# Performance work log

Measured on AMD Instinct MI355X. Metric: run time of the kernel, lower is better.

## Reference

```python
import math
import jax, jax.numpy as jnp
import numpy as np

TOP_K = 2
_GELU_C = math.sqrt(2.0 / math.pi)

def gelu_new(x):
    # NewGELU: tanh approximation identical to the torch module
    return 0.5 * x * (1.0 + jnp.tanh(_GELU_C * (x + 0.044715 * x * x * x)))

def setup_inputs() -> dict:
    key = jax.random.key(0)
    ks = jax.random.split(key, 6)
    B, T, C, E, H = 2, 2048, 1024, 8, 4096
    s_in = 1.0 / math.sqrt(C)
    s_hid = 1.0 / math.sqrt(H)
    return {
        "x": jax.random.normal(ks[0], (B, T, C), dtype=jnp.float32),
        "router_w": jax.random.normal(ks[1], (E, C), dtype=jnp.float32) * s_in,
        "w_fc": jax.random.normal(ks[2], (E, C, H), dtype=jnp.float32) * s_in,
        "b_fc": jax.random.normal(ks[3], (E, H), dtype=jnp.float32) * 0.02,
        "w_proj": jax.random.normal(ks[4], (E, H, C), dtype=jnp.float32) * s_hid,
        "b_proj": jax.random.normal(ks[5], (E, C), dtype=jnp.float32) * 0.02,
    }

def reference(x, router_w, w_fc, b_fc, w_proj, b_proj):
    B, T, C = x.shape
    E = router_w.shape[0]
    N = B * T
    xf = x.reshape(N, C)
    # Router: Linear(C, E, bias=False), softmax, top-k, renormalize
    logits = xf @ router_w.T                              # [N, E]
    probs = jax.nn.softmax(logits, axis=-1)
    topk_probs, topk_idx = jax.lax.top_k(probs, TOP_K)    # [N, K]
    topk_probs = topk_probs / jnp.sum(topk_probs, axis=-1, keepdims=True)
    # Dense combine weights: zero for unselected experts -> same math as
    # gather/FFN/index_add over selected tokens (dropout=0).
    combine = jnp.zeros((N, E), dtype=x.dtype).at[
        jnp.arange(N)[:, None], topk_idx].add(topk_probs)  # [N, E]
    # Expert FFN applied per expert (batched GEMMs)
    h = gelu_new(jnp.einsum('nc,ech->neh', xf, w_fc) + b_fc)      # [N, E, H]
    out = jnp.einsum('neh,ehc->nec', h, w_proj) + b_proj          # [N, E, C]
    y = jnp.einsum('nec,ne->nc', out, combine)                    # [N, C]
    return y.reshape(B, T, C)
```

## Files before the change

### kernel.cpp

```cpp
#include <hip/hip_runtime.h>


#define NTOK  4096
#define CDIM  1024
#define HDIM  4096
#define NEXP  8
#define NPC   9216
#define MAXMT 72
#define KB_C  32
#define KB_H  128
#define KSPLIT 2

#define FC_TOTAL (32 * MAXMT)
#define FC_CHUNK (FC_TOTAL / 8)
#define PJ_TOTAL (8 * MAXMT * KSPLIT)
#define PJ_CHUNK (PJ_TOTAL / 8)

typedef _Float16 half8 __attribute__((ext_vector_type(8)));
typedef float    f32x4 __attribute__((ext_vector_type(4)));

#define ASYNC_CP16(gp, lp)                                                         \
  __builtin_amdgcn_global_load_lds(                                                \
      (const __attribute__((address_space(1))) unsigned int*)(gp),                 \
      (__attribute__((address_space(3))) unsigned int*)(lp), 16, 0, 0)

#define STAGE(kb, LA, LB, BSTRIDE)                                                 \
  {                                                                                \
    const char* ga_ = gA0 + (size_t)(kb) * (NPC * 64) + soff;                      \
    const char* gb_ = gB0 + (size_t)(kb) * ((BSTRIDE) * 64) + soff;                \
    ASYNC_CP16(ga_,        LA);                                                    \
    ASYNC_CP16(ga_ + 1024, LA + 1024);                                             \
    ASYNC_CP16(gb_,        LB);                                                    \
    ASYNC_CP16(gb_ + 1024, LB + 1024);                                             \
  }

#define WAITV(N) asm volatile("s_waitcnt vmcnt(" #N ")" ::: "memory")
#define BAR()    __builtin_amdgcn_s_barrier()
#define SCHED0() __builtin_amdgcn_sched_barrier(0)

__device__ __forceinline__ void compute_step(
    const _Float16* __restrict__ AS, const _Float16* __restrict__ BS,
    int wm, int wn, int l16, int lq, f32x4 (&acc)[4][4])
{
    half8 af[4], bfv[4];
    #pragma unroll
    for (int i = 0; i < 4; ++i) af[i]  = *(const half8*)&AS[(wm + i * 16 + l16) * 32 + lq * 8];
    #pragma unroll
    for (int j = 0; j < 4; ++j) bfv[j] = *(const half8*)&BS[(wn + j * 16 + l16) * 32 + lq * 8];
    #pragma unroll
    for (int i = 0; i < 4; ++i)
        #pragma unroll
        for (int j = 0; j < 4; ++j)
            acc[i][j] = __builtin_amdgcn_mfma_f32_16x16x32_f16(af[i], bfv[j], acc[i][j], 0, 0, 0);
}

#define PIPE_LOOP(kb_beg, kb_end, BSTRIDE)                                         \
  {                                                                                \
    STAGE((kb_beg),     lA0, lB0, BSTRIDE);                                        \
    STAGE((kb_beg) + 1, lA1, lB1, BSTRIDE);                                        \
    for (int t = (kb_beg); t + 2 < (kb_end); t += 2) {                             \
        WAITV(4); BAR();                                                           \
        compute_step(As0, Bs0, wm, wn, l16, lq, acc);                              \
        SCHED0(); BAR();                                                           \
        STAGE(t + 2, lA0, lB0, BSTRIDE);                                           \
        WAITV(4); BAR();                                                           \
        compute_step(As1, Bs1, wm, wn, l16, lq, acc);                              \
        SCHED0(); BAR();                                                           \
        STAGE(t + 3, lA1, lB1, BSTRIDE);                                           \
    }                                                                              \
    WAITV(4); BAR();                                                               \
    compute_step(As0, Bs0, wm, wn, l16, lq, acc);                                  \
    SCHED0(); BAR();                                                               \
    WAITV(0); BAR();                                                               \
    compute_step(As1, Bs1, wm, wn, l16, lq, acc);                                  \
  }

__device__ __forceinline__ float gelu_new(float x) {
    const float c = 0.7978845608028654f;
    float u = c * (x + 0.044715f * x * x * x);
    return x / (1.0f + __expf(-2.0f * u));
}


__global__ void zero_init(unsigned int* __restrict__ pairs,
                          unsigned int* __restrict__ counts) {
    int i = blockIdx.x * 256 + threadIdx.x;
    if (i < 2 * NPC) pairs[i] = 0u;
    if (i < NEXP) counts[i] = 0u;
}


__global__ __launch_bounds__(256) void router_kernel(
    const float* __restrict__ x, const float* __restrict__ rw,
    int* __restrict__ tok_e, float* __restrict__ tok_w, int* __restrict__ counts)
{
    int wave = threadIdx.x >> 6, lane = threadIdx.x & 63;
    int n = blockIdx.x * 4 + wave;
    const float* xr = x + (size_t)n * CDIM;
    float acc[NEXP];
    #pragma unroll
    for (int e = 0; e < NEXP; ++e) acc[e] = 0.f;
    for (int c = lane; c < CDIM; c += 64) {
        float xv = xr[c];
        #pragma unroll
        for (int e = 0; e < NEXP; ++e) acc[e] = fmaf(xv, rw[e * CDIM + c], acc[e]);
    }
    #pragma unroll
    for (int e = 0; e < NEXP; ++e) {
        float v = acc[e];
        #pragma unroll
        for (int off = 32; off > 0; off >>= 1) v += __shfl_down(v, off);
        acc[e] = v;
    }
    if (lane == 0) {
        float l0 = -3.0e38f, l1 = -3.0e38f; int b0 = 0, b1 = 0;
        #pragma unroll
        for (int e = 0; e < NEXP; ++e) {
            float v = acc[e];
            if (v > l0)      { l1 = l0; b1 = b0; l0 = v; b0 = e; }
            else if (v > l1) { l1 = v; b1 = e; }
        }
        float t  = expf(l1 - l0);
        float w0 = 1.f / (1.f + t);
        float w1 = t  / (1.f + t);
        tok_e[n * 2]     = b0;  tok_e[n * 2 + 1] = b1;
        tok_w[n * 2]     = w0;  tok_w[n * 2 + 1] = w1;
        atomicAdd(&counts[b0], 1);
        atomicAdd(&counts[b1], 1);
    }
}

__global__ void plan_kernel(const int* __restrict__ counts, int* __restrict__ cursors,
                            int* __restrict__ mtiles, int* __restrict__ tile_expert)
{
    if (threadIdx.x == 0 && blockIdx.x == 0) {
        int b = 0;
        for (int e = 0; e < NEXP; ++e) {
            cursors[e] = b;
            int tiles = (counts[e] + 127) >> 7;
            for (int t = 0; t < tiles; ++t) tile_expert[(b >> 7) + t] = e;
            b += tiles << 7;
        }
        *mtiles = b >> 7;
        for (int t = b >> 7; t < MAXMT; ++t) tile_expert[t] = 0;
    }
}

__global__ void assign_kernel(const int* __restrict__ tok_e, const float* __restrict__ tok_w,
                              int* __restrict__ cursors,
                              int* __restrict__ pair_tok, float* __restrict__ pair_gate)
{
    int n = blockIdx.x * 256 + threadIdx.x;
    #pragma unroll
    for (int k = 0; k < 2; ++k) {
        int e = tok_e[n * 2 + k];
        int slot = atomicAdd(&cursors[e], 1);
        pair_tok[slot]  = n;
        pair_gate[slot] = tok_w[n * 2 + k];
    }
}


__global__ __launch_bounds__(256) void gather_x_kernel(
    const float* __restrict__ x, const int* __restrict__ pair_tok,
    _Float16* __restrict__ xg)
{
    int o = blockIdx.x * 256 + threadIdx.x;
    int kb   = o / (NPC * 4);
    int rem  = o - kb * (NPC * 4);
    int slot = rem >> 2;
    int c    = (rem & 3) * 8;
    int tok  = pair_tok[slot];
    const float* src = x + (size_t)tok * CDIM + kb * 32 + c;
    float4 a = *(const float4*)src;
    float4 b = *(const float4*)(src + 4);
    half8 h;
    h[0] = (_Float16)a.x; h[1] = (_Float16)a.y; h[2] = (_Float16)a.z; h[3] = (_Float16)a.w;
    h[4] = (_Float16)b.x; h[5] = (_Float16)b.y; h[6] = (_Float16)b.z; h[7] = (_Float16)b.w;
    *(half8*)(xg + ((size_t)kb * NPC + slot) * 32 + c) = h;
}


__global__ __launch_bounds__(256) void transpose_cvt_kernel(
    const float* __restrict__ w, _Float16* __restrict__ wt, int K, int N)
{
    __shared__ float tile[32][68];
    const int e = blockIdx.z, k0 = blockIdx.y * 32, n0 = blockIdx.x * 64;
    const float* src = w + ((size_t)e * K + k0) * N + n0;
    const int t = threadIdx.x;
    #pragma unroll
    for (int f = t; f < 512; f += 256) {
        int k = f >> 4, nc = (f & 15) * 4;
        *(float4*)&tile[k][nc] = *(const float4*)(src + (size_t)k * N + nc);
    }
    __syncthreads();
    int n = t >> 2, c2 = (t & 3) * 8;
    half8 h;
    #pragma unroll
    for (int q = 0; q < 8; ++q) h[q] = (_Float16)tile[c2 + q][n];
    int KB = K >> 5;
    _Float16* dst = wt + (((size_t)e * KB + (k0 >> 5)) * N + (n0 + n)) * 32 + c2;
    *(half8*)dst = h;
}


__global__ __launch_bounds__(256) void gemm_fc_kernel(
    const _Float16* __restrict__ xg,
    const _Float16* __restrict__ wt,
    const float*    __restrict__ b_fc,
    const int*      __restrict__ tile_expert,
    const int*      __restrict__ mtiles,
    _Float16*       __restrict__ hb)
{
    const unsigned flat = blockIdx.y * 32u + blockIdx.x;
    const unsigned logical = (flat & 7u) * FC_CHUNK + (flat >> 3);
    const int nt = logical & 31;
    const int mt = logical >> 5;
    if (mt >= *mtiles) return;
    const int e  = tile_expert[mt];
    const int m0 = mt << 7, n0 = nt << 7;

    __shared__ _Float16 As0[128 * 32], Bs0[128 * 32];
    __shared__ _Float16 As1[128 * 32], Bs1[128 * 32];

    const int tid = threadIdx.x;
    const int lane = tid & 63, wv = tid >> 6;
    const int wm = (wv >> 1) * 64, wn = (wv & 1) * 64;
    const int l16 = lane & 15, lq = lane >> 4;

    const char* gA0 = (const char*)xg + (size_t)m0 * 64;
    const char* gB0 = (const char*)wt + ((size_t)e * KB_C * HDIM + n0) * 64;
    const int soff = wv * 2048 + lane * 16;
    char* lA0 = (char*)As0 + wv * 2048;  char* lB0 = (char*)Bs0 + wv * 2048;
    char* lA1 = (char*)As1 + wv * 2048;  char* lB1 = (char*)Bs1 + wv * 2048;

    f32x4 acc[4][4];
    #pragma unroll
    for (int i = 0; i < 4; ++i)
        #pragma unroll
        for (int j = 0; j < 4; ++j) { acc[i][j][0]=0.f; acc[i][j][1]=0.f; acc[i][j][2]=0.f; acc[i][j][3]=0.f; }

    PIPE_LOOP(0, KB_C, HDIM);

    float bias[4];
    #pragma unroll
    for (int j = 0; j < 4; ++j) bias[j] = b_fc[e * HDIM + n0 + wn + j * 16 + l16];
    #pragma unroll
    for (int i = 0; i < 4; ++i) {
        #pragma unroll
        for (int r = 0; r < 4; ++r) {
            int slot = m0 + wm + i * 16 + lq * 4 + r;
            #pragma unroll
            for (int j = 0; j < 4; ++j) {
                int n = n0 + wn + j * 16 + l16;
                float v = gelu_new(acc[i][j][r] + bias[j]);
                hb[((size_t)(n >> 5) * NPC + slot) * 32 + (n & 31)] = (_Float16)v;
            }
        }
    }
}


__global__ __launch_bounds__(256) void gemm_proj_kernel(
    const _Float16* __restrict__ hb,
    const _Float16* __restrict__ wt,
    const float*    __restrict__ b_proj,
    const int*      __restrict__ pair_tok,
    const float*    __restrict__ pair_gate,
    const int*      __restrict__ tile_expert,
    const int*      __restrict__ mtiles,
    float*          __restrict__ y)
{
    const unsigned flat = (blockIdx.z * MAXMT + blockIdx.y) * 8u + blockIdx.x;
    const unsigned logical = (flat & 7u) * PJ_CHUNK + (flat >> 3);
    const int nt = logical & 7;
    const unsigned t2 = logical >> 3;
    const int mt = t2 % MAXMT;
    const int ks = t2 / MAXMT;
    if (mt >= *mtiles) return;
    const int e  = tile_expert[mt];
    const int m0 = mt << 7, n0 = nt << 7;

    __shared__ _Float16 As0[128 * 32], Bs0[128 * 32];
    __shared__ _Float16 As1[128 * 32], Bs1[128 * 32];

    const int tid = threadIdx.x;
    const int lane = tid & 63, wv = tid >> 6;
    const int wm = (wv >> 1) * 64, wn = (wv & 1) * 64;
    const int l16 = lane & 15, lq = lane >> 4;

    const char* gA0 = (const char*)hb + (size_t)m0 * 64;
    const char* gB0 = (const char*)wt + ((size_t)e * KB_H * CDIM + n0) * 64;
    const int soff = wv * 2048 + lane * 16;
    char* lA0 = (char*)As0 + wv * 2048;  char* lB0 = (char*)Bs0 + wv * 2048;
    char* lA1 = (char*)As1 + wv * 2048;  char* lB1 = (char*)Bs1 + wv * 2048;

    f32x4 acc[4][4];
    #pragma unroll
    for (int i = 0; i < 4; ++i)
        #pragma unroll
        for (int j = 0; j < 4; ++j) { acc[i][j][0]=0.f; acc[i][j][1]=0.f; acc[i][j][2]=0.f; acc[i][j][3]=0.f; }

    const int kb_beg = ks * (KB_H / KSPLIT);
    const int kb_end = kb_beg + (KB_H / KSPLIT);
    PIPE_LOOP(kb_beg, kb_end, CDIM);

    float bias[4];
    #pragma unroll
    for (int j = 0; j < 4; ++j)
        bias[j] = (ks == 0) ? b_proj[e * CDIM + n0 + wn + j * 16 + l16] : 0.0f;
    #pragma unroll
    for (int i = 0; i < 4; ++i) {
        #pragma unroll
        for (int r = 0; r < 4; ++r) {
            int slot = m0 + wm + i * 16 + lq * 4 + r;
            float g  = pair_gate[slot];
            if (g != 0.0f) {
                int tok = pair_tok[slot];
                float* dst = y + (size_t)tok * CDIM + n0 + wn + l16;
                #pragma unroll
                for (int j = 0; j < 4; ++j)
                    atomicAdd(&dst[j * 16], (acc[i][j][r] + bias[j]) * g);
            }
        }
    }
}


extern "C" void kernel_launch(void* const* d_in, const int* in_sizes, int n_in,
                              void* d_out, int out_size, void* d_ws, size_t ws_size,
                              hipStream_t stream) {
    const float* x   = (const float*)d_in[0];
    const float* rw  = (const float*)d_in[1];
    const float* wfc = (const float*)d_in[2];
    const float* bfc = (const float*)d_in[3];
    const float* wpj = (const float*)d_in[4];
    const float* bpj = (const float*)d_in[5];
    float* y = (float*)d_out;

    char* ws = (char*)d_ws;
    _Float16* xg  = (_Float16*)(ws);
    _Float16* hb  = (_Float16*)(ws + 18874368);
    _Float16* wt  = (_Float16*)(ws + 94371840);
    char* meta = ws + 161480704;
    int*   pair_tok    = (int*)  (meta);
    float* pair_gate   = (float*)(meta + 36864);
    int*   tok_e       = (int*)  (meta + 73728);
    float* tok_w       = (float*)(meta + 106496);
    int*   counts      = (int*)  (meta + 139264);
    int*   cursors     = counts + 8;
    int*   mtiles      = cursors + 8;
    int*   tile_expert = mtiles + 2;

    hipMemsetAsync(y, 0, (size_t)NTOK * CDIM * sizeof(float), stream);
    zero_init<<<(2 * NPC) / 256, 256, 0, stream>>>((unsigned int*)pair_tok,
                                                   (unsigned int*)counts);

    router_kernel<<<1024, 256, 0, stream>>>(x, rw, tok_e, tok_w, counts);
    plan_kernel<<<1, 64, 0, stream>>>(counts, cursors, mtiles, tile_expert);
    assign_kernel<<<16, 256, 0, stream>>>(tok_e, tok_w, cursors, pair_tok, pair_gate);
    gather_x_kernel<<<KB_C * NPC * 4 / 256, 256, 0, stream>>>(x, pair_tok, xg);

    transpose_cvt_kernel<<<dim3(HDIM / 64, CDIM / 32, NEXP), 256, 0, stream>>>(wfc, wt, CDIM, HDIM);
    gemm_fc_kernel<<<dim3(HDIM / 128, MAXMT), 256, 0, stream>>>(
        xg, wt, bfc, tile_expert, mtiles, hb);

    transpose_cvt_kernel<<<dim3(CDIM / 64, HDIM / 32, NEXP), 256, 0, stream>>>(wpj, wt, HDIM, CDIM);
    gemm_proj_kernel<<<dim3(CDIM / 128, MAXMT, KSPLIT), 256, 0, stream>>>(
        hb, wt, bpj, pair_tok, pair_gate, tile_expert, mtiles, y);
}
```

Before: 697.2 us.

## Replace split-K atomic scatter in proj GEMM with per-slot store and combine kernel

The projection GEMM no longer uses split-K or float atomics into y. Each slot's output is now written as fp16 to a scratch buffer that reuses the xg region, and a new combine kernel reads each token's two expert rows, applies the gate weights and writes y directly. This removes the memset of y and the atomic contention. The transpose kernel also now handles 64 rows of K per block. The costs are fewer proj blocks (less parallelism), an extra pass over a scratch buffer, and fp16 rounding of expert outputs before they are combined.

```diff
diff --git a/kernel.cpp b/kernel.cpp
--- a/kernel.cpp
+++ b/kernel.cpp
@@ -9,11 +9,10 @@
 #define MAXMT 72
 #define KB_C  32
 #define KB_H  128
-#define KSPLIT 2
 
 #define FC_TOTAL (32 * MAXMT)
 #define FC_CHUNK (FC_TOTAL / 8)
-#define PJ_TOTAL (8 * MAXMT * KSPLIT)
+#define PJ_TOTAL (8 * MAXMT)
 #define PJ_CHUNK (PJ_TOTAL / 8)
 
 typedef _Float16 half8 __attribute__((ext_vector_type(8)));
@@ -82,10 +81,10 @@
 }
 
 
-__global__ void zero_init(unsigned int* __restrict__ pairs,
+__global__ void zero_init(unsigned int* __restrict__ pair_tok,
                           unsigned int* __restrict__ counts) {
     int i = blockIdx.x * 256 + threadIdx.x;
-    if (i < 2 * NPC) pairs[i] = 0u;
+    if (i < NPC) pair_tok[i] = 0u;
     if (i < NEXP) counts[i] = 0u;
 }
 
@@ -146,17 +145,17 @@
     }
 }
 
-__global__ void assign_kernel(const int* __restrict__ tok_e, const float* __restrict__ tok_w,
+__global__ void assign_kernel(const int* __restrict__ tok_e,
                               int* __restrict__ cursors,
-                              int* __restrict__ pair_tok, float* __restrict__ pair_gate)
+                              int* __restrict__ pair_tok, int* __restrict__ tok_slot)
 {
     int n = blockIdx.x * 256 + threadIdx.x;
     #pragma unroll
     for (int k = 0; k < 2; ++k) {
         int e = tok_e[n * 2 + k];
         int slot = atomicAdd(&cursors[e], 1);
-        pair_tok[slot]  = n;
-        pair_gate[slot] = tok_w[n * 2 + k];
+        pair_tok[slot]     = n;
+        tok_slot[n * 2 + k] = slot;
     }
 }
 
@@ -184,23 +183,26 @@
 __global__ __launch_bounds__(256) void transpose_cvt_kernel(
     const float* __restrict__ w, _Float16* __restrict__ wt, int K, int N)
 {
-    __shared__ float tile[32][68];
-    const int e = blockIdx.z, k0 = blockIdx.y * 32, n0 = blockIdx.x * 64;
+    __shared__ float tile[64][69];
+    const int e = blockIdx.z, k0 = blockIdx.y * 64, n0 = blockIdx.x * 64;
     const float* src = w + ((size_t)e * K + k0) * N + n0;
     const int t = threadIdx.x;
     #pragma unroll
-    for (int f = t; f < 512; f += 256) {
+    for (int q = 0; q < 4; ++q) {
+        int f = t + 256 * q;
         int k = f >> 4, nc = (f & 15) * 4;
         *(float4*)&tile[k][nc] = *(const float4*)(src + (size_t)k * N + nc);
     }
     __syncthreads();
-    int n = t >> 2, c2 = (t & 3) * 8;
-    half8 h;
-    #pragma unroll
-    for (int q = 0; q < 8; ++q) h[q] = (_Float16)tile[c2 + q][n];
-    int KB = K >> 5;
-    _Float16* dst = wt + (((size_t)e * KB + (k0 >> 5)) * N + (n0 + n)) * 32 + c2;
-    *(half8*)dst = h;
+    const int n = t >> 2, c2 = (t & 3) * 8;
+    const int KB = K >> 5, kb0 = k0 >> 5;
+    #pragma unroll
+    for (int h2 = 0; h2 < 2; ++h2) {
+        half8 h;
+        #pragma unroll
+        for (int q = 0; q < 8; ++q) h[q] = (_Float16)tile[h2 * 32 + c2 + q][n];
+        *(half8*)(wt + (((size_t)e * KB + kb0 + h2) * N + (n0 + n)) * 32 + c2) = h;
+    }
 }
 
 
@@ -265,18 +267,14 @@
     const _Float16* __restrict__ hb,
     const _Float16* __restrict__ wt,
     const float*    __restrict__ b_proj,
-    const int*      __restrict__ pair_tok,
-    const float*    __restrict__ pair_gate,
     const int*      __restrict__ tile_expert,
     const int*      __restrict__ mtiles,
-    float*          __restrict__ y)
-{
-    const unsigned flat = (blockIdx.z * MAXMT + blockIdx.y) * 8u + blockIdx.x;
+    _Float16*       __restrict__ out_s)
+{
+    const unsigned flat = blockIdx.y * 8u + blockIdx.x;
     const unsigned logical = (flat & 7u) * PJ_CHUNK + (flat >> 3);
     const int nt = logical & 7;
-    const unsigned t2 = logical >> 3;
-    const int mt = t2 % MAXMT;
-    const int ks = t2 / MAXMT;
+    const int mt = logical >> 3;
     if (mt >= *mtiles) return;
     const int e  = tile_expert[mt];
     const int m0 = mt << 7, n0 = nt << 7;
@@ -301,29 +299,49 @@
         #pragma unroll
         for (int j = 0; j < 4; ++j) { acc[i][j][0]=0.f; acc[i][j][1]=0.f; acc[i][j][2]=0.f; acc[i][j][3]=0.f; }
 
-    const int kb_beg = ks * (KB_H / KSPLIT);
-    const int kb_end = kb_beg + (KB_H / KSPLIT);
-    PIPE_LOOP(kb_beg, kb_end, CDIM);
+    PIPE_LOOP(0, KB_H, CDIM);
 
     float bias[4];
     #pragma unroll
-    for (int j = 0; j < 4; ++j)
-        bias[j] = (ks == 0) ? b_proj[e * CDIM + n0 + wn + j * 16 + l16] : 0.0f;
+    for (int j = 0; j < 4; ++j) bias[j] = b_proj[e * CDIM + n0 + wn + j * 16 + l16];
     #pragma unroll
     for (int i = 0; i < 4; ++i) {
         #pragma unroll
         for (int r = 0; r < 4; ++r) {
             int slot = m0 + wm + i * 16 + lq * 4 + r;
-            float g  = pair_gate[slot];
-            if (g != 0.0f) {
-                int tok = pair_tok[slot];
-                float* dst = y + (size_t)tok * CDIM + n0 + wn + l16;
-                #pragma unroll
-                for (int j = 0; j < 4; ++j)
-                    atomicAdd(&dst[j * 16], (acc[i][j][r] + bias[j]) * g);
-            }
+            _Float16* dst = out_s + (size_t)slot * CDIM + n0 + wn + l16;
+            #pragma unroll
+            for (int j = 0; j < 4; ++j)
+                dst[j * 16] = (_Float16)(acc[i][j][r] + bias[j]);
         }
     }
+}
+
+
+__global__ __launch_bounds__(256) void combine_kernel(
+    const _Float16* __restrict__ out_s,
+    const int*      __restrict__ tok_slot,
+    const float*    __restrict__ tok_w,
+    float*          __restrict__ y)
+{
+    int idx = blockIdx.x * 256 + threadIdx.x;
+    int n  = idx >> 7;
+    int c8 = (idx & 127) * 8;
+    int s0 = tok_slot[n * 2], s1 = tok_slot[n * 2 + 1];
+    float g0 = tok_w[n * 2], g1 = tok_w[n * 2 + 1];
+    half8 o0 = *(const half8*)(out_s + (size_t)s0 * CDIM + c8);
+    half8 o1 = *(const half8*)(out_s + (size_t)s1 * CDIM + c8);
+    float4 a, b;
+    a.x = g0 * (float)o0[0] + g1 * (float)o1[0];
+    a.y = g0 * (float)o0[1] + g1 * (float)o1[1];
+    a.z = g0 * (float)o0[2] + g1 * (float)o1[2];
+    a.w = g0 * (float)o0[3] + g1 * (float)o1[3];
+    b.x = g0 * (float)o0[4] + g1 * (float)o1[4];
+    b.y = g0 * (float)o0[5] + g1 * (float)o1[5];
+    b.z = g0 * (float)o0[6] + g1 * (float)o1[6];
+    b.w = g0 * (float)o0[7] + g1 * (float)o1[7];
+    *(float4*)(y + (size_t)n * CDIM + c8)     = a;
+    *(float4*)(y + (size_t)n * CDIM + c8 + 4) = b;
 }
 
 
@@ -340,11 +358,12 @@
 
     char* ws = (char*)d_ws;
     _Float16* xg  = (_Float16*)(ws);
+    _Float16* out_s = (_Float16*)(ws);
     _Float16* hb  = (_Float16*)(ws + 18874368);
     _Float16* wt  = (_Float16*)(ws + 94371840);
     char* meta = ws + 161480704;
     int*   pair_tok    = (int*)  (meta);
-    float* pair_gate   = (float*)(meta + 36864);
+    int*   tok_slot    = (int*)  (meta + 36864);
     int*   tok_e       = (int*)  (meta + 73728);
     float* tok_w       = (float*)(meta + 106496);
     int*   counts      = (int*)  (meta + 139264);
@@ -352,20 +371,20 @@
     int*   mtiles      = cursors + 8;
     int*   tile_expert = mtiles + 2;
 
-    hipMemsetAsync(y, 0, (size_t)NTOK * CDIM * sizeof(float), stream);
-    zero_init<<<(2 * NPC) / 256, 256, 0, stream>>>((unsigned int*)pair_tok,
-                                                   (unsigned int*)counts);
+    zero_init<<<(NPC + 255) / 256, 256, 0, stream>>>((unsigned int*)pair_tok,
+                                                     (unsigned int*)counts);
 
     router_kernel<<<1024, 256, 0, stream>>>(x, rw, tok_e, tok_w, counts);
     plan_kernel<<<1, 64, 0, stream>>>(counts, cursors, mtiles, tile_expert);
-    assign_kernel<<<16, 256, 0, stream>>>(tok_e, tok_w, cursors, pair_tok, pair_gate);
+    assign_kernel<<<16, 256, 0, stream>>>(tok_e, cursors, pair_tok, tok_slot);
     gather_x_kernel<<<KB_C * NPC * 4 / 256, 256, 0, stream>>>(x, pair_tok, xg);
 
-    transpose_cvt_kernel<<<dim3(HDIM / 64, CDIM / 32, NEXP), 256, 0, stream>>>(wfc, wt, CDIM, HDIM);
+    transpose_cvt_kernel<<<dim3(HDIM / 64, CDIM / 64, NEXP), 256, 0, stream>>>(wfc, wt, CDIM, HDIM);
     gemm_fc_kernel<<<dim3(HDIM / 128, MAXMT), 256, 0, stream>>>(
         xg, wt, bfc, tile_expert, mtiles, hb);
 
-    transpose_cvt_kernel<<<dim3(CDIM / 64, HDIM / 32, NEXP), 256, 0, stream>>>(wpj, wt, HDIM, CDIM);
-    gemm_proj_kernel<<<dim3(CDIM / 128, MAXMT, KSPLIT), 256, 0, stream>>>(
-        hb, wt, bpj, pair_tok, pair_gate, tile_expert, mtiles, y);
-}
+    transpose_cvt_kernel<<<dim3(CDIM / 64, HDIM / 64, NEXP), 256, 0, stream>>>(wpj, wt, HDIM, CDIM);
+    gemm_proj_kernel<<<dim3(CDIM / 128, MAXMT), 256, 0, stream>>>(
+        hb, wt, bpj, tile_expert, mtiles, out_s);
+    combine_kernel<<<NTOK * (CDIM / 8) / 256, 256, 0, stream>>>(out_s, tok_slot, tok_w, y);
+}
```

After: 681.5 us. 2.2% less time.
